# Kernel tuning notes

Hardware: AMD Instinct MI355X
Metric: run time of the kernel (lower is better)

The kernel has to match this reference:

```python
import jax, jax.numpy as jnp
import numpy as np

M, K, N = 1024, 32, 2048   # feature dim, components, samples
N_ITERS = 1500             # projected-gradient iterations for NNLS


def setup_inputs() -> dict:
    key = jax.random.key(0)
    k1, k2 = jax.random.split(key)
    # Nonnegative data matrix X (m, n) and nonnegative dictionary theta (m, k),
    # matching torch.abs(torch.rand(m, k)) init in the module.
    X = jax.random.uniform(k1, (M, N), dtype=jnp.float32)
    theta = jax.random.uniform(k2, (M, K), dtype=jnp.float32)
    return {"X": X, "theta": theta}


def _nnls_batched(theta, X):
    """Solve beta[:, l] = argmin_{b>=0} ||theta @ b - X[:, l]||^2 for all columns.

    Same optimization problem scipy.optimize.nnls solves per column in the
    original module, here solved for all n columns simultaneously with
    projected gradient descent (convex problem -> same minimizer; projection
    yields exact zeros on the inactive set, matching NNLS support structure).
    """
    G = theta.T @ theta                      # (k, k) Gram matrix
    L = jnp.linalg.eigvalsh(G)[-1] + 1e-6    # Lipschitz constant of the gradient
    T = theta.T @ X                          # (k, n)
    B0 = jnp.zeros_like(T)

    def body(_, B):
        return jnp.maximum(B - (G @ B - T) / L, 0.0)

    return jax.lax.fori_loop(0, N_ITERS, body, B0)


def reference(X, theta):
    # Module clamps theta to be nonnegative before the factorization solve.
    theta = jnp.maximum(theta, 0.0)
    return _nnls_batched(theta, X)   # beta: (k, n)
```

## Files before the change

### kernel.cpp

```cpp
#include <hip/hip_runtime.h>
#include <math.h>

#define M_DIM 1024
#define K_DIM 32
#define N_DIM 2048
#define ACC_ITERS 350
#define POLISH_ITERS 50
#define POW_ITERS 12

#define G_OFF    0
#define THC_OFF  2048
#define T_OFF    36864

__device__ __forceinline__ float bcast_lane(float x, int lane) {
    return __int_as_float(__builtin_amdgcn_readlane(__float_as_int(x), lane));
}

__global__ void __launch_bounds__(256) kA(const float* __restrict__ theta,
                                          float* __restrict__ G,
                                          float* __restrict__ thc) {
    int tid = threadIdx.x;
    int bid = blockIdx.x;

    if (bid >= 32) {
        int e = (bid - 32) * 256 + tid;
        thc[e] = fmaxf(theta[e], 0.f);
        return;
    }

    __shared__ float red[8][32];
    int i  = bid;
    int j  = tid & 31;
    int ms = tid >> 5;
    float p = 0.f;
    for (int mq = 0; mq < 128; ++mq) {
        int m = ms * 128 + mq;
        float a = fmaxf(theta[m * K_DIM + i], 0.f);
        float b = fmaxf(theta[m * K_DIM + j], 0.f);
        p = fmaf(a, b, p);
    }
    red[ms][j] = p;
    __syncthreads();
    if (ms == 0) {
        float s = p;
        for (int q = 1; q < 8; ++q) s += red[q][j];
        G[i * 32 + j] = s;
    }
}

__global__ void __launch_bounds__(256) kT(const float* __restrict__ X,
                                          const float* __restrict__ thc,
                                          float* __restrict__ T) {
    int tid = threadIdx.x;
    int c   = blockIdx.x * 256 + tid;
    int m0  = blockIdx.y * 128;

    float acc[32];
#pragma unroll
    for (int i = 0; i < 32; ++i) acc[i] = 0.f;

    for (int m = 0; m < 128; ++m) {
        int row = m0 + m;
        float x = X[row * N_DIM + c];
        const float4* t4 = reinterpret_cast<const float4*>(thc + row * K_DIM);
#pragma unroll
        for (int q = 0; q < 8; ++q) {
            float4 v = t4[q];
            acc[4 * q + 0] = fmaf(v.x, x, acc[4 * q + 0]);
            acc[4 * q + 1] = fmaf(v.y, x, acc[4 * q + 1]);
            acc[4 * q + 2] = fmaf(v.z, x, acc[4 * q + 2]);
            acc[4 * q + 3] = fmaf(v.w, x, acc[4 * q + 3]);
        }
    }
#pragma unroll
    for (int i = 0; i < 32; ++i) atomicAdd(&T[i * N_DIM + c], acc[i]);
}

__global__ void __launch_bounds__(256, 2) kPGD(const float* __restrict__ G,
                                               const float* __restrict__ T,
                                               float* __restrict__ out) {
    __shared__ float Gsh[32][33];
    __shared__ float lamsh, betash;
    int tid = threadIdx.x;
#pragma unroll
    for (int q = 0; q < 4; ++q) {
        int e = q * 256 + tid;
        Gsh[e >> 5][e & 31] = G[e];
    }
    __syncthreads();

    int i  = tid & 31;
    int wv = tid >> 6;
    int col = blockIdx.x * 4 + wv;

    float g[32];
#pragma unroll
    for (int j = 0; j < 32; ++j) g[j] = Gsh[i][j];

    if (tid < 64) {
        float v = 1.f, lam = 1.f;
        for (int p = 0; p < POW_ITERS; ++p) {
            float w = 0.f;
#pragma unroll
            for (int j = 0; j < 32; ++j) w = fmaf(g[j], bcast_lane(v, j), w);
            float n2 = w * w;
#pragma unroll
            for (int m = 1; m < 32; m <<= 1) n2 += __shfl_xor(n2, m, 32);
            lam = sqrtf(n2);
            v = w / lam;
        }
        float d = Gsh[i][i];
#pragma unroll
        for (int m = 1; m < 32; m <<= 1) d += __shfl_xor(d, m, 32);
        if (tid == 0) {
            float L  = lam + 1e-6f;
            float mu = 0.25f * (d - lam) * (1.0f / 31.0f);
            mu = fmaxf(mu, 1e-3f * L);
            float sL = sqrtf(L), sm = sqrtf(mu);
            lamsh  = L;
            betash = (sL - sm) / (sL + sm);
        }
    }
    __syncthreads();

    float invL = 1.0f / lamsh;
    float beta = betash;

    float ar[32];
#pragma unroll
    for (int j = 0; j < 32; ++j) {
        ar[j] = ((j == i) ? 1.0f : 0.0f) - g[j] * invL;
        asm volatile("" : "+v"(ar[j]));
    }
    float t = T[i * N_DIM + col] * invL;

    __syncthreads();
#pragma unroll
    for (int q = 0; q < 4; ++q) {
        int e = q * 256 + tid;
        Gsh[e >> 5][e & 31] = 0.f;
    }
    __syncthreads();
    t = fmaf(Gsh[i][(tid * 7) & 31], 0.0f, t);

    float y = 0.f, bprev = 0.f;
    for (int it = 0; it < ACC_ITERS; ++it) {
        float bj[32];
#pragma unroll
        for (int j = 0; j < 32; ++j) bj[j] = bcast_lane(y, j);
        float a0 = t, a1 = 0.f, a2 = 0.f, a3 = 0.f;
#pragma unroll
        for (int j = 0; j < 32; j += 4) {
            a0 = fmaf(ar[j + 0], bj[j + 0], a0);
            a1 = fmaf(ar[j + 1], bj[j + 1], a1);
            a2 = fmaf(ar[j + 2], bj[j + 2], a2);
            a3 = fmaf(ar[j + 3], bj[j + 3], a3);
        }
        float w = fmaxf((a0 + a1) + (a2 + a3), 0.f);
        y = fmaf(beta, w - bprev, w);
        bprev = w;
    }
    for (int it = 0; it < POLISH_ITERS; ++it) {
        float bj[32];
#pragma unroll
        for (int j = 0; j < 32; ++j) bj[j] = bcast_lane(y, j);
        float a0 = t, a1 = 0.f, a2 = 0.f, a3 = 0.f;
#pragma unroll
        for (int j = 0; j < 32; j += 4) {
            a0 = fmaf(ar[j + 0], bj[j + 0], a0);
            a1 = fmaf(ar[j + 1], bj[j + 1], a1);
            a2 = fmaf(ar[j + 2], bj[j + 2], a2);
            a3 = fmaf(ar[j + 3], bj[j + 3], a3);
        }
        y = fmaxf((a0 + a1) + (a2 + a3), 0.f);
    }

    if ((tid & 32) == 0) out[i * N_DIM + col] = y;
}

extern "C" void kernel_launch(void* const* d_in, const int* in_sizes, int n_in,
                              void* d_out, int out_size, void* d_ws, size_t ws_size,
                              hipStream_t stream) {
    const float* X     = (const float*)d_in[0];
    const float* theta = (const float*)d_in[1];
    float* ws  = (float*)d_ws;
    float* G   = ws + G_OFF;
    float* thc = ws + THC_OFF;
    float* T   = ws + T_OFF;

    hipMemsetAsync(T, 0, (size_t)K_DIM * N_DIM * sizeof(float), stream);
    kA<<<160, 256, 0, stream>>>(theta, G, thc);
    kT<<<dim3(8, 8), 256, 0, stream>>>(X, thc, T);
    kPGD<<<512, 256, 0, stream>>>(G, T, (float*)d_out);
}
```

Before: 181.9 us.

## Fuse Gram, projection and PGD kernels into one cooperative kernel with grid sync

Replaces the memset and three kernel launches with a single cooperative launch. Blocks 0-31 compute the Gram matrix and blocks 32-95 compute T, reducing partial sums in LDS with plain stores instead of global atomics. A grid-wide sync then lets all 512 blocks run the accelerated PGD solve. This removes per-launch overhead, the memset and the clamped-theta copy, but it needs all 512 blocks co-resident and pays for a grid barrier. The T computation also runs on only 64 blocks.

```diff
diff --git a/kernel.cpp b/kernel.cpp
--- a/kernel.cpp
+++ b/kernel.cpp
@@ -1,5 +1,8 @@
 #include <hip/hip_runtime.h>
+#include <hip/hip_cooperative_groups.h>
 #include <math.h>
+
+namespace cg = cooperative_groups;
 
 #define M_DIM 1024
 #define K_DIM 32
@@ -8,94 +11,86 @@
 #define POLISH_ITERS 50
 #define POW_ITERS 12
 
-#define G_OFF    0
-#define THC_OFF  2048
-#define T_OFF    36864
+#define G_OFF 0
+#define T_OFF 2048
 
 __device__ __forceinline__ float bcast_lane(float x, int lane) {
     return __int_as_float(__builtin_amdgcn_readlane(__float_as_int(x), lane));
 }
 
-__global__ void __launch_bounds__(256) kA(const float* __restrict__ theta,
-                                          float* __restrict__ G,
-                                          float* __restrict__ thc) {
+__global__ void __launch_bounds__(256, 2) kFused(const float* __restrict__ X,
+                                                 const float* __restrict__ theta,
+                                                 float* __restrict__ G,
+                                                 float* __restrict__ T,
+                                                 float* __restrict__ out) {
+    __shared__ float lds[8192];
     int tid = threadIdx.x;
     int bid = blockIdx.x;
 
-    if (bid >= 32) {
-        int e = (bid - 32) * 256 + tid;
-        thc[e] = fmaxf(theta[e], 0.f);
-        return;
-    }
-
-    __shared__ float red[8][32];
-    int i  = bid;
-    int j  = tid & 31;
-    int ms = tid >> 5;
-    float p = 0.f;
-    for (int mq = 0; mq < 128; ++mq) {
-        int m = ms * 128 + mq;
-        float a = fmaxf(theta[m * K_DIM + i], 0.f);
-        float b = fmaxf(theta[m * K_DIM + j], 0.f);
-        p = fmaf(a, b, p);
-    }
-    red[ms][j] = p;
-    __syncthreads();
-    if (ms == 0) {
-        float s = p;
-        for (int q = 1; q < 8; ++q) s += red[q][j];
-        G[i * 32 + j] = s;
-    }
-}
-
-__global__ void __launch_bounds__(256) kT(const float* __restrict__ X,
-                                          const float* __restrict__ thc,
-                                          float* __restrict__ T) {
-    int tid = threadIdx.x;
-    int c   = blockIdx.x * 256 + tid;
-    int m0  = blockIdx.y * 128;
-
-    float acc[32];
+    if (bid < 32) {
+        int i = bid, j = tid & 31, ms = tid >> 5;
+        float p = 0.f;
+        for (int mq = 0; mq < 128; ++mq) {
+            int m = ms * 128 + mq;
+            float a = fmaxf(theta[m * K_DIM + i], 0.f);
+            float b = fmaxf(theta[m * K_DIM + j], 0.f);
+            p = fmaf(a, b, p);
+        }
+        lds[ms * 32 + j] = p;
+        __syncthreads();
+        if (ms == 0) {
+            float s = p;
+            for (int q = 1; q < 8; ++q) s += lds[q * 32 + j];
+            G[i * 32 + j] = s;
+        }
+    } else if (bid < 96) {
+        int tb = bid - 32;
+        int lc = tid & 31;
+        int c  = tb * 32 + lc;
+        int ms = tid >> 5;
+        float acc[32];
 #pragma unroll
-    for (int i = 0; i < 32; ++i) acc[i] = 0.f;
-
-    for (int m = 0; m < 128; ++m) {
-        int row = m0 + m;
-        float x = X[row * N_DIM + c];
-        const float4* t4 = reinterpret_cast<const float4*>(thc + row * K_DIM);
+        for (int q = 0; q < 32; ++q) acc[q] = 0.f;
+        for (int mq = 0; mq < 128; ++mq) {
+            int m = ms * 128 + mq;
+            float x = X[m * N_DIM + c];
+            const float4* t4 = reinterpret_cast<const float4*>(theta + m * K_DIM);
 #pragma unroll
-        for (int q = 0; q < 8; ++q) {
-            float4 v = t4[q];
-            acc[4 * q + 0] = fmaf(v.x, x, acc[4 * q + 0]);
-            acc[4 * q + 1] = fmaf(v.y, x, acc[4 * q + 1]);
-            acc[4 * q + 2] = fmaf(v.z, x, acc[4 * q + 2]);
-            acc[4 * q + 3] = fmaf(v.w, x, acc[4 * q + 3]);
+            for (int q = 0; q < 8; ++q) {
+                float4 v = t4[q];
+                acc[4 * q + 0] = fmaf(fmaxf(v.x, 0.f), x, acc[4 * q + 0]);
+                acc[4 * q + 1] = fmaf(fmaxf(v.y, 0.f), x, acc[4 * q + 1]);
+                acc[4 * q + 2] = fmaf(fmaxf(v.z, 0.f), x, acc[4 * q + 2]);
+                acc[4 * q + 3] = fmaf(fmaxf(v.w, 0.f), x, acc[4 * q + 3]);
+            }
+        }
+#pragma unroll
+        for (int q = 0; q < 32; ++q) lds[ms * 1024 + q * 32 + lc] = acc[q];
+        __syncthreads();
+        for (int q = 0; q < 4; ++q) {
+            int e = q * 256 + tid;
+            float s = 0.f;
+            for (int s8 = 0; s8 < 8; ++s8) s += lds[s8 * 1024 + e];
+            T[(e >> 5) * N_DIM + tb * 32 + (e & 31)] = s;
         }
     }
-#pragma unroll
-    for (int i = 0; i < 32; ++i) atomicAdd(&T[i * N_DIM + c], acc[i]);
-}
+    __threadfence();
+    cg::this_grid().sync();
 
-__global__ void __launch_bounds__(256, 2) kPGD(const float* __restrict__ G,
-                                               const float* __restrict__ T,
-                                               float* __restrict__ out) {
-    __shared__ float Gsh[32][33];
-    __shared__ float lamsh, betash;
-    int tid = threadIdx.x;
 #pragma unroll
     for (int q = 0; q < 4; ++q) {
         int e = q * 256 + tid;
-        Gsh[e >> 5][e & 31] = G[e];
+        lds[(e >> 5) * 33 + (e & 31)] = G[e];
     }
     __syncthreads();
 
     int i  = tid & 31;
     int wv = tid >> 6;
-    int col = blockIdx.x * 4 + wv;
+    int col = bid * 4 + wv;
 
     float g[32];
 #pragma unroll
-    for (int j = 0; j < 32; ++j) g[j] = Gsh[i][j];
+    for (int j = 0; j < 32; ++j) g[j] = lds[i * 33 + j];
 
     if (tid < 64) {
         float v = 1.f, lam = 1.f;
@@ -109,7 +104,7 @@
             lam = sqrtf(n2);
             v = w / lam;
         }
-        float d = Gsh[i][i];
+        float d = g[i];
 #pragma unroll
         for (int m = 1; m < 32; m <<= 1) d += __shfl_xor(d, m, 32);
         if (tid == 0) {
@@ -117,14 +112,14 @@
             float mu = 0.25f * (d - lam) * (1.0f / 31.0f);
             mu = fmaxf(mu, 1e-3f * L);
             float sL = sqrtf(L), sm = sqrtf(mu);
-            lamsh  = L;
-            betash = (sL - sm) / (sL + sm);
+            lds[1100] = L;
+            lds[1101] = (sL - sm) / (sL + sm);
         }
     }
     __syncthreads();
 
-    float invL = 1.0f / lamsh;
-    float beta = betash;
+    float invL = 1.0f / lds[1100];
+    float beta = lds[1101];
 
     float ar[32];
 #pragma unroll
@@ -136,12 +131,12 @@
 
     __syncthreads();
 #pragma unroll
-    for (int q = 0; q < 4; ++q) {
+    for (int q = 0; q < 5; ++q) {
         int e = q * 256 + tid;
-        Gsh[e >> 5][e & 31] = 0.f;
+        if (e < 1102) lds[e] = 0.f;
     }
     __syncthreads();
-    t = fmaf(Gsh[i][(tid * 7) & 31], 0.0f, t);
+    t = fmaf(lds[i * 33 + ((tid * 7) & 31)], 0.0f, t);
 
     float y = 0.f, bprev = 0.f;
     for (int it = 0; it < ACC_ITERS; ++it) {
@@ -185,11 +180,10 @@
     const float* theta = (const float*)d_in[1];
     float* ws  = (float*)d_ws;
     float* G   = ws + G_OFF;
-    float* thc = ws + THC_OFF;
     float* T   = ws + T_OFF;
+    float* out = (float*)d_out;
 
-    hipMemsetAsync(T, 0, (size_t)K_DIM * N_DIM * sizeof(float), stream);
-    kA<<<160, 256, 0, stream>>>(theta, G, thc);
-    kT<<<dim3(8, 8), 256, 0, stream>>>(X, thc, T);
-    kPGD<<<512, 256, 0, stream>>>(G, T, (float*)d_out);
+    void* args[] = {(void*)&X, (void*)&theta, (void*)&G, (void*)&T, (void*)&out};
+    hipLaunchCooperativeKernel((const void*)kFused, dim3(512), dim3(256),
+                               args, 0, stream);
 }
```

After: 306.3 us. 1.68x slower.
